# Kernel optimization log

Hardware: AMD Instinct MI355X
Metric: run time of the kernel (lower is better)

Reference implementation:

```python
import jax, jax.numpy as jnp
import numpy as np


def setup_inputs() -> dict:
    key = jax.random.key(0)
    k1, k2, k3 = jax.random.split(key, 3)
    B, S, H, Dk = 4, 1024, 16, 4
    E = H * Dk
    return {
        "x": jax.random.normal(k1, (B, S, E), dtype=jnp.float32),
        "theta": jax.random.normal(k2, (Dk,), dtype=jnp.float32),  # heads[0] RY params, shared by all heads (bug in source reproduced)
        "W": jax.random.normal(k3, (E, E), dtype=jnp.float32) / np.sqrt(E),
        "b": jnp.zeros((E,), dtype=jnp.float32),
    }


def reference(x, theta, W, b):
    # x: [B, S, E], E = H * 4
    B, S, E = x.shape
    Dk = 4
    H = E // Dk
    inv_sqrt_dk = 1.0 / np.float32(np.sqrt(Dk))

    # 4-qubit circuit per token/head, no entangling gates -> each wire independent:
    #   |0> --RX(x_i)--RY(theta_i)--  <PauliZ> = cos(theta_i) * cos(x_i)
    # (exact closed form of the torchquantum statevector simulation)
    # chunk along embed dim == reshape [B, S, H, Dk]
    proj = jnp.cos(x.reshape(B, S, H, Dk)) * jnp.cos(theta)  # theta broadcasts over wires
    proj = proj.transpose(0, 2, 1, 3)  # [B, H, S, Dk]

    scores = jnp.einsum('bhsd,bhtd->bhst', proj, proj) * inv_sqrt_dk  # [B, H, S, S]
    attn = jax.nn.softmax(scores, axis=-1)  # dropout = identity in eval mode
    out = jnp.einsum('bhst,bhtd->bhsd', attn, proj)  # [B, H, S, Dk]

    out = out.transpose(0, 2, 1, 3).reshape(B, S, E)  # [B, S, E]
    return out @ W.T + b
```

## Files before the change

kernel.cpp:

```cpp
#include <hip/hip_runtime.h>
#include <hip/hip_bf16.h>

#define SQ 1024
#define HH 16
#define DK 4
#define EE 64

using short8 = __attribute__((ext_vector_type(8))) short;
using f32x4  = __attribute__((ext_vector_type(4))) float;
using us4    = __attribute__((ext_vector_type(4))) unsigned short;
using us8    = __attribute__((ext_vector_type(8))) unsigned short;

static __device__ inline unsigned short f2bf(float f) {
  return __builtin_bit_cast(unsigned short, __float2bfloat16(f));
}

__global__ __launch_bounds__(512) void qattn_mfma(
    const float* __restrict__ x, const float* __restrict__ theta,
    float* __restrict__ y) {
  const int tid = threadIdx.x;
  const int quarter = blockIdx.x & 3;
  const int bh = blockIdx.x >> 2;
  const int hd = bh & (HH - 1);
  const int b = bh >> 4;

  __shared__ __align__(16) unsigned short afrag[32][16][8];
  __shared__ __align__(16) unsigned short vfrag[32][4][5][8];
  __shared__ __align__(16) unsigned short qfrag[256][4];
  __shared__ __align__(16) unsigned short zslot[8];

  const float4 th = *reinterpret_cast<const float4*>(theta);
  const float ct[4] = {__cosf(th.x), __cosf(th.y), __cosf(th.z), __cosf(th.w)};
  const float sc = 0.5f * 1.4426950408889634f;
  const int q_lo = quarter * 256;

  if (tid < 8) zslot[tid] = 0;
#pragma unroll
  for (int k = 0; k < 2; ++k) {
    const int e = tid + k * 512;
    vfrag[e >> 5][(e >> 3) & 3][4][e & 7] = 0x3F80;
  }

  const float* xb = x + ((size_t)b * SQ) * EE + hd * DK;
#pragma unroll
  for (int k = 0; k < 2; ++k) {
    const int t = tid + k * 512;
    const float4 v = *reinterpret_cast<const float4*>(xb + (size_t)t * EE);
    const float p[4] = {__cosf(v.x) * ct[0], __cosf(v.y) * ct[1],
                        __cosf(v.z) * ct[2], __cosf(v.w) * ct[3]};
    unsigned short pb[4], qb[4];
#pragma unroll
    for (int d = 0; d < 4; ++d) {
      pb[d] = f2bf(p[d]);
      qb[d] = f2bf(p[d] * sc);
    }
    const int c = t >> 5, tl = t & 31, hq = tl >> 3, j = tl & 7;
    *reinterpret_cast<us4*>(&afrag[c][4 * hq + (j & 3)][(j >= 4) ? 4 : 0]) =
        (us4){pb[0], pb[1], pb[2], pb[3]};
#pragma unroll
    for (int n = 0; n < 4; ++n) vfrag[c][hq][n][j] = pb[n];
    const int ql = t - q_lo;
    if ((unsigned)ql < 256u)
      *reinterpret_cast<us4*>(&qfrag[ql][0]) = (us4){qb[0], qb[1], qb[2], qb[3]};
  }
  __syncthreads();

  const int lane = tid & 63;
  const int wid = tid >> 6;
  const int n = lane & 15, hg = lane >> 4;

  short8 qfA = {0, 0, 0, 0, 0, 0, 0, 0}, qfB = qfA;
  {
    const unsigned short* qa = (lane < 16) ? &qfrag[wid * 32 + n][0] : &zslot[0];
    const unsigned short* qb2 = (lane < 16) ? &qfrag[wid * 32 + 16 + n][0] : &zslot[0];
    const us4 ta = *reinterpret_cast<const us4*>(qa);
    const us4 tb = *reinterpret_cast<const us4*>(qb2);
#pragma unroll
    for (int i = 0; i < 4; ++i) { qfA[i] = (short)ta[i]; qfB[i] = (short)tb[i]; }
  }

  const unsigned short* aptr = (lane < 16) ? &afrag[0][n][0] : &zslot[0];
  const int astep = (lane < 16) ? 128 : 0;
  const unsigned short* vptr = (n <= 4) ? &vfrag[0][hg][n][0] : &zslot[0];
  const int vstep = (n <= 4) ? 160 : 0;

  f32x4 accA = {0.f, 0.f, 0.f, 0.f}, accB = accA;
  const f32x4 zero = {0.f, 0.f, 0.f, 0.f};

#pragma unroll 2
  for (int c = 0; c < 32; ++c) {
    const us8 av = *reinterpret_cast<const us8*>(aptr + c * astep);
    const short8 A1 = {(short)av[0], (short)av[1], (short)av[2], (short)av[3],
                       0, 0, 0, 0};
    const short8 A2 = {(short)av[4], (short)av[5], (short)av[6], (short)av[7],
                       0, 0, 0, 0};
    const f32x4 s1A = __builtin_amdgcn_mfma_f32_16x16x32_bf16(A1, qfA, zero, 0, 0, 0);
    const f32x4 s2A = __builtin_amdgcn_mfma_f32_16x16x32_bf16(A2, qfA, zero, 0, 0, 0);
    const f32x4 s1B = __builtin_amdgcn_mfma_f32_16x16x32_bf16(A1, qfB, zero, 0, 0, 0);
    const f32x4 s2B = __builtin_amdgcn_mfma_f32_16x16x32_bf16(A2, qfB, zero, 0, 0, 0);

    short8 PA_A, PA_B;
#pragma unroll
    for (int r = 0; r < 4; ++r) {
      PA_A[r]     = (short)f2bf(__builtin_amdgcn_exp2f(s1A[r]));
      PA_A[r + 4] = (short)f2bf(__builtin_amdgcn_exp2f(s2A[r]));
      PA_B[r]     = (short)f2bf(__builtin_amdgcn_exp2f(s1B[r]));
      PA_B[r + 4] = (short)f2bf(__builtin_amdgcn_exp2f(s2B[r]));
    }

    const us8 vv = *reinterpret_cast<const us8*>(vptr + c * vstep);
    const short8 VB = __builtin_bit_cast(short8, vv);
    accA = __builtin_amdgcn_mfma_f32_16x16x32_bf16(PA_A, VB, accA, 0, 0, 0);
    accB = __builtin_amdgcn_mfma_f32_16x16x32_bf16(PA_B, VB, accB, 0, 0, 0);
  }

#pragma unroll
  for (int half = 0; half < 2; ++half) {
    const f32x4 acc = half ? accB : accA;
    const int qbase = q_lo + wid * 32 + half * 16;
#pragma unroll
    for (int r = 0; r < 4; ++r) {
      const float den = __shfl(acc[r], (lane & 48) | 4, 64);
      const float val = acc[r] * (1.0f / den);
      if (n < 4) {
        y[((size_t)(b * SQ + qbase + 4 * hg + r)) * EE + hd * DK + n] = val;
      }
    }
  }
}

__global__ __launch_bounds__(256) void proj_kernel(
    const float* __restrict__ y, const float* __restrict__ W,
    const float* __restrict__ bias, float* __restrict__ out) {
  const int tid = threadIdx.x;
  __shared__ float Wt[EE][EE + 1];
  __shared__ float yt[16][EE];

  const float4* W4 = reinterpret_cast<const float4*>(W);
#pragma unroll
  for (int k = 0; k < 4; ++k) {
    const int i4 = tid + k * 256;
    const float4 w = W4[i4];
    const int e = i4 >> 4;
    const int j = (i4 & 15) * 4;
    Wt[j + 0][e] = w.x; Wt[j + 1][e] = w.y;
    Wt[j + 2][e] = w.z; Wt[j + 3][e] = w.w;
  }
  const size_t tok0 = (size_t)blockIdx.x * 16;
  {
    const float4 v = reinterpret_cast<const float4*>(y + tok0 * EE)[tid];
    *reinterpret_cast<float4*>(&yt[tid >> 4][(tid & 15) * 4]) = v;
  }
  __syncthreads();

  const int e = tid & 63;
  const int t0 = tid >> 6;
  const float bv = bias[e];
  float acc[4] = {bv, bv, bv, bv};
#pragma unroll
  for (int j = 0; j < EE; ++j) {
    const float w = Wt[j][e];
#pragma unroll
    for (int k = 0; k < 4; ++k) acc[k] += yt[t0 + 4 * k][j] * w;
  }
#pragma unroll
  for (int k = 0; k < 4; ++k) {
    out[(tok0 + t0 + 4 * k) * EE + e] = acc[k];
  }
}

extern "C" void kernel_launch(void* const* d_in, const int* in_sizes, int n_in,
                              void* d_out, int out_size, void* d_ws, size_t ws_size,
                              hipStream_t stream) {
  const float* x     = (const float*)d_in[0];
  const float* theta = (const float*)d_in[1];
  const float* W     = (const float*)d_in[2];
  const float* bias  = (const float*)d_in[3];
  float* out = (float*)d_out;
  float* y   = (float*)d_ws;

  qattn_mfma<<<256, 512, 0, stream>>>(x, theta, y);
  proj_kernel<<<256, 256, 0, stream>>>(y, W, bias, out);
}
```

Baseline: 19.20 us.

## Use 1024-thread attention blocks with one query tile per wave; vectorize projection

The attention kernel now launches 1024 threads per block, so each of 16 waves handles a single 16-query tile instead of two. The x staging loop collapses to one token per thread. This gives more waves for latency hiding and halves per-wave serial MFMA/exp work, at the cost of re-reading the same LDS K/V fragments from twice as many waves. The projection kernel is also reworked: each thread computes 4 outputs for one token using float4 LDS reads of padded W and y tiles, and writes them with a single vector store.

```diff
diff --git a/kernel.cpp b/kernel.cpp
--- a/kernel.cpp
+++ b/kernel.cpp
@@ -15,7 +15,7 @@
   return __builtin_bit_cast(unsigned short, __float2bfloat16(f));
 }
 
-__global__ __launch_bounds__(512) void qattn_mfma(
+__global__ __launch_bounds__(1024) void qattn_mfma(
     const float* __restrict__ x, const float* __restrict__ theta,
     float* __restrict__ y) {
   const int tid = threadIdx.x;
@@ -35,16 +35,11 @@
   const int q_lo = quarter * 256;
 
   if (tid < 8) zslot[tid] = 0;
-#pragma unroll
-  for (int k = 0; k < 2; ++k) {
-    const int e = tid + k * 512;
-    vfrag[e >> 5][(e >> 3) & 3][4][e & 7] = 0x3F80;
-  }
+  vfrag[tid >> 5][(tid >> 3) & 3][4][tid & 7] = 0x3F80;
 
   const float* xb = x + ((size_t)b * SQ) * EE + hd * DK;
-#pragma unroll
-  for (int k = 0; k < 2; ++k) {
-    const int t = tid + k * 512;
+  {
+    const int t = tid;
     const float4 v = *reinterpret_cast<const float4*>(xb + (size_t)t * EE);
     const float p[4] = {__cosf(v.x) * ct[0], __cosf(v.y) * ct[1],
                         __cosf(v.z) * ct[2], __cosf(v.w) * ct[3]};
@@ -58,7 +53,7 @@
     *reinterpret_cast<us4*>(&afrag[c][4 * hq + (j & 3)][(j >= 4) ? 4 : 0]) =
         (us4){pb[0], pb[1], pb[2], pb[3]};
 #pragma unroll
-    for (int n = 0; n < 4; ++n) vfrag[c][hq][n][j] = pb[n];
+    for (int nn = 0; nn < 4; ++nn) vfrag[c][hq][nn][j] = pb[nn];
     const int ql = t - q_lo;
     if ((unsigned)ql < 256u)
       *reinterpret_cast<us4*>(&qfrag[ql][0]) = (us4){qb[0], qb[1], qb[2], qb[3]};
@@ -69,14 +64,13 @@
   const int wid = tid >> 6;
   const int n = lane & 15, hg = lane >> 4;
 
-  short8 qfA = {0, 0, 0, 0, 0, 0, 0, 0}, qfB = qfA;
+  short8 qf = {0, 0, 0, 0, 0, 0, 0, 0};
   {
-    const unsigned short* qa = (lane < 16) ? &qfrag[wid * 32 + n][0] : &zslot[0];
-    const unsigned short* qb2 = (lane < 16) ? &qfrag[wid * 32 + 16 + n][0] : &zslot[0];
+    const unsigned short* qa =
+        (lane < 16) ? &qfrag[wid * 16 + n][0] : &zslot[0];
     const us4 ta = *reinterpret_cast<const us4*>(qa);
-    const us4 tb = *reinterpret_cast<const us4*>(qb2);
 #pragma unroll
-    for (int i = 0; i < 4; ++i) { qfA[i] = (short)ta[i]; qfB[i] = (short)tb[i]; }
+    for (int i = 0; i < 4; ++i) qf[i] = (short)ta[i];
   }
 
   const unsigned short* aptr = (lane < 16) ? &afrag[0][n][0] : &zslot[0];
@@ -84,47 +78,38 @@
   const unsigned short* vptr = (n <= 4) ? &vfrag[0][hg][n][0] : &zslot[0];
   const int vstep = (n <= 4) ? 160 : 0;
 
-  f32x4 accA = {0.f, 0.f, 0.f, 0.f}, accB = accA;
+  f32x4 acc = {0.f, 0.f, 0.f, 0.f};
   const f32x4 zero = {0.f, 0.f, 0.f, 0.f};
 
-#pragma unroll 2
+#pragma unroll 4
   for (int c = 0; c < 32; ++c) {
     const us8 av = *reinterpret_cast<const us8*>(aptr + c * astep);
     const short8 A1 = {(short)av[0], (short)av[1], (short)av[2], (short)av[3],
                        0, 0, 0, 0};
     const short8 A2 = {(short)av[4], (short)av[5], (short)av[6], (short)av[7],
                        0, 0, 0, 0};
-    const f32x4 s1A = __builtin_amdgcn_mfma_f32_16x16x32_bf16(A1, qfA, zero, 0, 0, 0);
-    const f32x4 s2A = __builtin_amdgcn_mfma_f32_16x16x32_bf16(A2, qfA, zero, 0, 0, 0);
-    const f32x4 s1B = __builtin_amdgcn_mfma_f32_16x16x32_bf16(A1, qfB, zero, 0, 0, 0);
-    const f32x4 s2B = __builtin_amdgcn_mfma_f32_16x16x32_bf16(A2, qfB, zero, 0, 0, 0);
+    const f32x4 s1 = __builtin_amdgcn_mfma_f32_16x16x32_bf16(A1, qf, zero, 0, 0, 0);
+    const f32x4 s2 = __builtin_amdgcn_mfma_f32_16x16x32_bf16(A2, qf, zero, 0, 0, 0);
 
-    short8 PA_A, PA_B;
+    short8 PA;
 #pragma unroll
     for (int r = 0; r < 4; ++r) {
-      PA_A[r]     = (short)f2bf(__builtin_amdgcn_exp2f(s1A[r]));
-      PA_A[r + 4] = (short)f2bf(__builtin_amdgcn_exp2f(s2A[r]));
-      PA_B[r]     = (short)f2bf(__builtin_amdgcn_exp2f(s1B[r]));
-      PA_B[r + 4] = (short)f2bf(__builtin_amdgcn_exp2f(s2B[r]));
+      PA[r]     = (short)f2bf(__builtin_amdgcn_exp2f(s1[r]));
+      PA[r + 4] = (short)f2bf(__builtin_amdgcn_exp2f(s2[r]));
     }
 
     const us8 vv = *reinterpret_cast<const us8*>(vptr + c * vstep);
     const short8 VB = __builtin_bit_cast(short8, vv);
-    accA = __builtin_amdgcn_mfma_f32_16x16x32_bf16(PA_A, VB, accA, 0, 0, 0);
-    accB = __builtin_amdgcn_mfma_f32_16x16x32_bf16(PA_B, VB, accB, 0, 0, 0);
+    acc = __builtin_amdgcn_mfma_f32_16x16x32_bf16(PA, VB, acc, 0, 0, 0);
   }
 
+  const int qbase = q_lo + wid * 16;
 #pragma unroll
-  for (int half = 0; half < 2; ++half) {
-    const f32x4 acc = half ? accB : accA;
-    const int qbase = q_lo + wid * 32 + half * 16;
-#pragma unroll
-    for (int r = 0; r < 4; ++r) {
-      const float den = __shfl(acc[r], (lane & 48) | 4, 64);
-      const float val = acc[r] * (1.0f / den);
-      if (n < 4) {
-        y[((size_t)(b * SQ + qbase + 4 * hg + r)) * EE + hd * DK + n] = val;
-      }
+  for (int r = 0; r < 4; ++r) {
+    const float den = __shfl(acc[r], (lane & 48) | 4, 64);
+    const float val = acc[r] * (1.0f / den);
+    if (n < 4) {
+      y[((size_t)(b * SQ + qbase + 4 * hg + r)) * EE + hd * DK + n] = val;
     }
   }
 }
@@ -133,8 +118,8 @@
     const float* __restrict__ y, const float* __restrict__ W,
     const float* __restrict__ bias, float* __restrict__ out) {
   const int tid = threadIdx.x;
-  __shared__ float Wt[EE][EE + 1];
-  __shared__ float yt[16][EE];
+  __shared__ float Wt[EE][68];
+  __shared__ float yt[16][68];
 
   const float4* W4 = reinterpret_cast<const float4*>(W);
 #pragma unroll
@@ -142,9 +127,9 @@
     const int i4 = tid + k * 256;
     const float4 w = W4[i4];
     const int e = i4 >> 4;
-    const int j = (i4 & 15) * 4;
-    Wt[j + 0][e] = w.x; Wt[j + 1][e] = w.y;
-    Wt[j + 2][e] = w.z; Wt[j + 3][e] = w.w;
+    const int j0 = (i4 & 15) * 4;
+    Wt[j0 + 0][e] = w.x; Wt[j0 + 1][e] = w.y;
+    Wt[j0 + 2][e] = w.z; Wt[j0 + 3][e] = w.w;
   }
   const size_t tok0 = (size_t)blockIdx.x * 16;
   {
@@ -153,20 +138,20 @@
   }
   __syncthreads();
 
-  const int e = tid & 63;
-  const int t0 = tid >> 6;
-  const float bv = bias[e];
-  float acc[4] = {bv, bv, bv, bv};
+  const int t = tid >> 4;
+  const int eg = tid & 15;
+  const int e0 = eg * 4;
+  f32x4 acc = *reinterpret_cast<const f32x4*>(bias + e0);
 #pragma unroll
-  for (int j = 0; j < EE; ++j) {
-    const float w = Wt[j][e];
-#pragma unroll
-    for (int k = 0; k < 4; ++k) acc[k] += yt[t0 + 4 * k][j] * w;
+  for (int jq = 0; jq < 16; ++jq) {
+    const f32x4 yv = *reinterpret_cast<const f32x4*>(&yt[t][jq * 4]);
+    const f32x4 w0 = *reinterpret_cast<const f32x4*>(&Wt[jq * 4 + 0][e0]);
+    const f32x4 w1 = *reinterpret_cast<const f32x4*>(&Wt[jq * 4 + 1][e0]);
+    const f32x4 w2 = *reinterpret_cast<const f32x4*>(&Wt[jq * 4 + 2][e0]);
+    const f32x4 w3 = *reinterpret_cast<const f32x4*>(&Wt[jq * 4 + 3][e0]);
+    acc += yv[0] * w0 + yv[1] * w1 + yv[2] * w2 + yv[3] * w3;
   }
-#pragma unroll
-  for (int k = 0; k < 4; ++k) {
-    out[(tok0 + t0 + 4 * k) * EE + e] = acc[k];
-  }
+  *reinterpret_cast<f32x4*>(&out[((size_t)tok0 + t) * EE + e0]) = acc;
 }
 
 extern "C" void kernel_launch(void* const* d_in, const int* in_sizes, int n_in,
@@ -179,6 +164,6 @@
   float* out = (float*)d_out;
   float* y   = (float*)d_ws;
 
-  qattn_mfma<<<256, 512, 0, stream>>>(x, theta, y);
+  qattn_mfma<<<256, 1024, 0, stream>>>(x, theta, y);
   proj_kernel<<<256, 256, 0, stream>>>(y, W, bias, out);
 }
```

Result: slower. 19.66 us (+2.4%).
